# Kernel optimization log

Measured on AMD Instinct MI355X. Metric: run time of the kernel, lower is better.

The kernel has to match this reference:

```python
import jax, jax.numpy as jnp
import numpy as np

# Model dims
D = 2048        # hidden_size
H = 16          # num_heads
KVH = 8         # num_key_value_heads
DH = 128        # head_dim
NUM_SLOTS = 16  # state-cache slots
B = 4           # prefill segments (regularized ragged batch)
L = 2048        # tokens per segment
T = B * L
C = 64          # GLA chunk size (fused_chunk_gla)
NEG = -1e30


def setup_inputs() -> dict:
    key = jax.random.key(0)
    k0, k1, k2, k3 = jax.random.split(key, 4)
    hidden_states = jax.random.normal(k0, (T, D), jnp.float32)
    W_qkv = jax.random.normal(k1, (D, (H + 2 * KVH) * DH), jnp.float32) * 0.02
    b_qkv = jnp.zeros(((H + 2 * KVH) * DH,), jnp.float32)
    kv_cache = jax.random.normal(k2, (NUM_SLOTS, H, DH, DH), jnp.float32) * 0.1
    state_indices = jax.random.randint(k3, (B,), 0, NUM_SLOTS, jnp.int32)
    return {"hidden_states": hidden_states, "W_qkv": W_qkv, "b_qkv": b_qkv,
            "kv_cache": kv_cache, "state_indices": state_indices}


def _to_chunks(x):
    # [T, H, d] -> [n_chunks, B, C, H, d]
    return x.reshape(B, L // C, C, H, DH).transpose(1, 0, 2, 3, 4)


def _gla_chunk_body(mask):
    def body(S, inp):
        # S: [B,H,dk,dv]; qc/kc/vc/gc: [B,C,H,d]
        qc, kc, vc, gc = inp
        Bc = jnp.cumsum(gc, axis=1)                       # inclusive log-decay within chunk
        # inter-chunk: initial state decayed by exp(Bc)
        o_inter = jnp.einsum('bchk,bhkv->bchv', qc * jnp.exp(Bc), S)
        # intra-chunk causal scores: A_ij = sum_d q_i,d * exp(B_i - B_j)_d * k_j,d, j<=i
        diff = Bc[:, :, None] - Bc[:, None, :]            # [B,Ci,Cj,H,dk], <=0 on lower tri
        diff = jnp.where(mask[None, :, :, None, None], diff, NEG)
        A = jnp.einsum('bihk,bijhk,bjhk->bijh', qc, jnp.exp(diff), kc)
        o = o_inter + jnp.einsum('bijh,bjhv->bihv', A, vc)
        # state update: S' = diag(exp(B_last)) S + sum_j (k_j exp(B_last - B_j)) v_j^T
        b_last = Bc[:, -1]                                # [B,H,dk]
        kg = kc * jnp.exp(b_last[:, None] - Bc)
        S_new = S * jnp.exp(b_last)[..., None] + jnp.einsum('bchk,bchv->bhkv', kg, vc)
        return S_new, o
    return jax.checkpoint(body)


def _forward(hidden_states, W_qkv, b_qkv, kv_cache, state_indices):
    qkv = hidden_states @ W_qkv + b_qkv
    q = qkv[:, :H * DH].reshape(T, H, DH)
    k = qkv[:, H * DH:(H + KVH) * DH].reshape(T, KVH, DH)
    v = qkv[:, (H + KVH) * DH:].reshape(T, KVH, DH)
    n_rep = H // KVH
    k = jnp.repeat(k, n_rep, axis=1)                      # repeat_kv (3D branch)
    v = jnp.repeat(v, n_rep, axis=1)
    q = jax.nn.relu(q) * DH ** -0.5                       # q_feature_map + fused_chunk_gla scale
    k = jnp.minimum(jax.nn.sigmoid(k), 0.95)              # sigmoid + clamp(max=clamp_max)
    g = jnp.log1p(-k)                                     # (1 - k).log()

    S0 = kv_cache[state_indices]                          # [B,H,dk,dv] per-slot initial states
    mask = jnp.tril(jnp.ones((C, C), bool))
    _, o = jax.lax.scan(_gla_chunk_body(mask), S0,
                        (_to_chunks(q), _to_chunks(k), _to_chunks(v), _to_chunks(g)))
    # [n_chunks,B,C,H,dv] -> per-segment concat [T, H*dv]
    return o.transpose(1, 0, 2, 3, 4).reshape(T, H * DH)


def reference(hidden_states, W_qkv, b_qkv, kv_cache, state_indices):
    return _forward(hidden_states, W_qkv, b_qkv, kv_cache, state_indices)
```

## Files before the change

kernel.cpp:

```cpp
#include <hip/hip_runtime.h>
#include <hip/hip_bf16.h>
#include <math.h>

#define RSQRT_DH 0.08838834764831845f

typedef __attribute__((ext_vector_type(8))) short short8;
typedef __attribute__((ext_vector_type(4))) float floatx4;

static __device__ __forceinline__ float bf2f(unsigned short u) {
  return __uint_as_float(((unsigned int)u) << 16);
}
static __device__ __forceinline__ unsigned short f2bf(float f) {
  unsigned int x = __float_as_uint(f);
  return (unsigned short)((x + 0x7fffu + ((x >> 16) & 1u)) >> 16);
}
static __device__ __forceinline__ ushort4 f4bf(float a, float b, float c, float d) {
  ushort4 r; r.x = f2bf(a); r.y = f2bf(b); r.z = f2bf(c); r.w = f2bf(d); return r;
}
static __device__ __forceinline__ short8 ld8u(const unsigned short* p) {
  short4 a = *(const short4*)p;
  short4 b = *(const short4*)(p + 4);
  short8 r;
  r[0] = a.x; r[1] = a.y; r[2] = a.z; r[3] = a.w;
  r[4] = b.x; r[5] = b.y; r[6] = b.z; r[7] = b.w;
  return r;
}

__launch_bounds__(256)
__global__ void k_cvt(const float* __restrict__ in, unsigned short* __restrict__ out, int n4) {
  int i = blockIdx.x * 256 + threadIdx.x;
  if (i >= n4) return;
  float4 v = ((const float4*)in)[i];
  ((ushort4*)out)[i] = f4bf(v.x, v.y, v.z, v.w);
}

__launch_bounds__(256)
__global__ void k_cvt_wt(const float* __restrict__ W, unsigned short* __restrict__ Wt) {
  __shared__ float tile[32][33];
  int t = threadIdx.x;
  int c = t & 31, r = t >> 5;
  int bx = blockIdx.x, by = blockIdx.y;
#pragma unroll
  for (int j = 0; j < 4; ++j)
    tile[r + j * 8][c] = W[(size_t)(by * 32 + r + j * 8) * 4096 + bx * 32 + c];
  __syncthreads();
#pragma unroll
  for (int j = 0; j < 4; ++j)
    Wt[(size_t)(bx * 32 + r + j * 8) * 2048 + by * 32 + c] = f2bf(tile[c][r + j * 8]);
}

__launch_bounds__(256)
__global__ void k_gemm(const unsigned short* __restrict__ A,
                       const unsigned short* __restrict__ Bt,
                       const float* __restrict__ bias,
                       unsigned short* __restrict__ qb,
                       unsigned short* __restrict__ kb,
                       unsigned short* __restrict__ vb,
                       float* __restrict__ gf) {
  __shared__ unsigned short lds_a[128 * 64];
  __shared__ unsigned short lds_b[128 * 64];
  const int t = threadIdx.x;
  const int m0 = blockIdx.y * 128;
  const int n0 = blockIdx.x * 128;
  const int w = t >> 6, l = t & 63;
  const int wr = w >> 1, wc = w & 1;

  const int srow = l >> 3;
  const int scol = (l & 7) * 8;
  const unsigned short* agp = A + (size_t)(m0 + w * 8 + srow) * 2048 + scol;
  const unsigned short* bgp = Bt + (size_t)(n0 + w * 8 + srow) * 2048 + scol;

  floatx4 acc[4][4] = {};

  for (int kt = 0; kt < 2048; kt += 64) {
    __syncthreads();
#pragma unroll
    for (int it = 0; it < 4; ++it) {
      __builtin_amdgcn_global_load_lds(
          (const __attribute__((address_space(1))) void*)(agp + kt + (size_t)it * 32 * 2048),
          (__attribute__((address_space(3))) void*)(lds_a + (it * 32 + w * 8) * 64),
          16, 0, 0);
      __builtin_amdgcn_global_load_lds(
          (const __attribute__((address_space(1))) void*)(bgp + kt + (size_t)it * 32 * 2048),
          (__attribute__((address_space(3))) void*)(lds_b + (it * 32 + w * 8) * 64),
          16, 0, 0);
    }
    __syncthreads();
#pragma unroll
    for (int ks = 0; ks < 2; ++ks) {
      short8 af[4], bf[4];
      const int krow = ks * 32 + (l >> 4) * 8;
#pragma unroll
      for (int ti = 0; ti < 4; ++ti)
        af[ti] = *(const short8*)(lds_a + (wr * 64 + ti * 16 + (l & 15)) * 64 + krow);
#pragma unroll
      for (int tj = 0; tj < 4; ++tj)
        bf[tj] = *(const short8*)(lds_b + (wc * 64 + tj * 16 + (l & 15)) * 64 + krow);
#pragma unroll
      for (int ti = 0; ti < 4; ++ti)
#pragma unroll
        for (int tj = 0; tj < 4; ++tj)
          acc[ti][tj] = __builtin_amdgcn_mfma_f32_16x16x32_bf16(af[ti], bf[tj], acc[ti][tj], 0, 0, 0);
    }
  }
#pragma unroll
  for (int ti = 0; ti < 4; ++ti) {
#pragma unroll
    for (int tj = 0; tj < 4; ++tj) {
      const int n = n0 + wc * 64 + tj * 16 + (l & 15);
      const float bn = bias[n];
#pragma unroll
      for (int r = 0; r < 4; ++r) {
        const int m = m0 + wr * 64 + ti * 16 + ((l >> 4) * 4) + r;
        float val = acc[ti][tj][r] + bn;
        if (n < 2048) {
          qb[(size_t)m * 2048 + n] = f2bf(fmaxf(val, 0.f) * RSQRT_DH);
        } else if (n < 3072) {
          float s = 1.f / (1.f + __expf(-val));
          s = fminf(s, 0.95f);
          size_t idx = (size_t)m * 1024 + (n - 2048);
          kb[idx] = f2bf(s);
          gf[idx] = log1pf(-s);
        } else {
          vb[(size_t)m * 1024 + (n - 3072)] = f2bf(val);
        }
      }
    }
  }
}

__launch_bounds__(256)
__global__ void k_phaseA(const unsigned short* __restrict__ kb,
                         const unsigned short* __restrict__ vb,
                         const float* __restrict__ gf,
                         float* __restrict__ blast,
                         unsigned short* __restrict__ Pb) {
  __shared__ float sBc[64 * 128];
  __shared__ float sKg[64 * 128];
  const int t = threadIdx.x;
  const int chunk = blockIdx.x, chain = blockIdx.y;
  const int b = chain >> 4, h = chain & 15, kvh = h >> 1;
  const int t0 = b * 2048 + chunk * 64;

#pragma unroll
  for (int rep = 0; rep < 8; ++rep) {
    int e = rep * 256 + t;
    int i = e >> 5, d4 = e & 31;
    *(float4*)(sBc + i * 128 + d4 * 4) =
        *(const float4*)(gf + (size_t)(t0 + i) * 1024 + kvh * 128 + d4 * 4);
  }
  __syncthreads();
  if (t < 128) {
    float run = sBc[t];
    for (int i = 1; i < 64; ++i) { run += sBc[i * 128 + t]; sBc[i * 128 + t] = run; }
    blast[((size_t)chain * 32 + chunk) * 128 + t] = run;
  }
  __syncthreads();
#pragma unroll
  for (int rep = 0; rep < 32; ++rep) {
    int e = rep * 256 + t;
    int i = e >> 7, d = e & 127;
    float kk = bf2f(kb[(size_t)(t0 + i) * 1024 + kvh * 128 + d]);
    sKg[e] = kk * __expf(sBc[63 * 128 + d] - sBc[e]);
  }
  __syncthreads();
  const int kq = t >> 3, vq = t & 7;
  const int kd0 = kq * 4, vd0 = vq * 16;
  float acc[4][16] = {};
  const unsigned short* vrow = vb + (size_t)t0 * 1024 + kvh * 128 + vd0;
  for (int i = 0; i < 64; ++i) {
    float4 kg4 = *(const float4*)(sKg + i * 128 + kd0);
    float ka[4] = {kg4.x, kg4.y, kg4.z, kg4.w};
    ushort4 v0 = *(const ushort4*)(vrow + (size_t)i * 1024);
    ushort4 v1 = *(const ushort4*)(vrow + (size_t)i * 1024 + 4);
    ushort4 v2 = *(const ushort4*)(vrow + (size_t)i * 1024 + 8);
    ushort4 v3 = *(const ushort4*)(vrow + (size_t)i * 1024 + 12);
    float vf[16] = {bf2f(v0.x), bf2f(v0.y), bf2f(v0.z), bf2f(v0.w),
                    bf2f(v1.x), bf2f(v1.y), bf2f(v1.z), bf2f(v1.w),
                    bf2f(v2.x), bf2f(v2.y), bf2f(v2.z), bf2f(v2.w),
                    bf2f(v3.x), bf2f(v3.y), bf2f(v3.z), bf2f(v3.w)};
#pragma unroll
    for (int r = 0; r < 4; ++r)
#pragma unroll
      for (int j = 0; j < 16; ++j) acc[r][j] += ka[r] * vf[j];
  }
  size_t pbase = ((size_t)chain * 32 + chunk) * 16384;
#pragma unroll
  for (int r = 0; r < 4; ++r)
#pragma unroll
    for (int j4 = 0; j4 < 4; ++j4)
      *(ushort4*)(Pb + pbase + (size_t)(kd0 + r) * 128 + vd0 + j4 * 4) =
          f4bf(acc[r][j4 * 4], acc[r][j4 * 4 + 1], acc[r][j4 * 4 + 2], acc[r][j4 * 4 + 3]);
}

__launch_bounds__(256)
__global__ void k_scan(const float* __restrict__ kv_cache,
                       const int* __restrict__ sidx,
                       const float* __restrict__ blast,
                       const unsigned short* __restrict__ Pb,
                       unsigned short* __restrict__ Sb) {
  const int t = threadIdx.x;
  const int part = blockIdx.x;
  const int chain = blockIdx.y;
  const int b = chain >> 4, h = chain & 15;
  const int e0 = part * 1024 + t * 4;
  const int kd = e0 >> 7;
  const int slot = sidx[b];
  float4 s = *(const float4*)(kv_cache + ((size_t)slot * 16 + h) * 16384 + e0);
#pragma unroll 1
  for (int c = 0; c < 32; ++c) {
    *(ushort4*)(Sb + ((size_t)c * 64 + chain) * 16384 + e0) = f4bf(s.x, s.y, s.z, s.w);
    float eb = __expf(blast[((size_t)chain * 32 + c) * 128 + kd]);
    ushort4 p = *(const ushort4*)(Pb + ((size_t)chain * 32 + c) * 16384 + e0);
    s.x = s.x * eb + bf2f(p.x);
    s.y = s.y * eb + bf2f(p.y);
    s.z = s.z * eb + bf2f(p.z);
    s.w = s.w * eb + bf2f(p.w);
  }
}

__launch_bounds__(256)
__global__ void k_output(const unsigned short* __restrict__ qb,
                         const unsigned short* __restrict__ kb,
                         const unsigned short* __restrict__ vb,
                         const float* __restrict__ gf,
                         const unsigned short* __restrict__ Sb,
                         float* __restrict__ out) {
  __shared__ float sBc[64 * 128];
  __shared__ unsigned short sR3[11136];
  unsigned short* sA   = sR3;
  unsigned short* sKE  = sR3 + 4608;
  unsigned short* sQE2 = sR3 + 4608 + 4352;
  unsigned short* sQE0 = sR3;
  unsigned short* sSt  = sR3 + 4608;
  unsigned short* sVt  = sR3 + 4608;

  const int t = threadIdx.x;
  const int w = t >> 6, l = t & 63;
  const int lr = l & 15, quad = l >> 4;
  const int chunk = blockIdx.x, chain = blockIdx.y;
  const int b = chain >> 4, h = chain & 15, kvh = h >> 1;
  const int t0 = b * 2048 + chunk * 64;
  const size_t sbase = ((size_t)chunk * 64 + chain) * 16384;

#pragma unroll
  for (int rep = 0; rep < 8; ++rep) {
    int e = rep * 256 + t, i = e >> 5, d4 = e & 31;
    *(float4*)(sBc + i * 128 + d4 * 4) =
        *(const float4*)(gf + (size_t)(t0 + i) * 1024 + kvh * 128 + d4 * 4);
  }
  __syncthreads();
  if (t < 128) {
    float run = sBc[t];
#pragma unroll
    for (int i = 1; i < 64; ++i) { run += sBc[i * 128 + t]; sBc[i * 128 + t] = run; }
  }

  floatx4 o[8];
#pragma unroll
  for (int i = 0; i < 8; ++i) o[i] = 0.f;

#pragma unroll
  for (int kh = 0; kh < 2; ++kh) {
    __syncthreads();
#pragma unroll
    for (int rep = 0; rep < 2; ++rep) {
      int idx = rep * 256 + t;
      int i = idx >> 3, g = idx & 7;
      int k0 = kh * 64 + g * 8;
      short8 q8 = *(const short8*)(qb + (size_t)(t0 + i) * 2048 + h * 128 + k0);
      short8 r;
#pragma unroll
      for (int u = 0; u < 8; ++u)
        r[u] = (short)f2bf(bf2f((unsigned short)q8[u]) * __expf(sBc[i * 128 + k0 + u]));
      *(short8*)(sQE0 + i * 72 + g * 8) = r;
    }
#pragma unroll
    for (int vh = 0; vh < 2; ++vh) {
      __syncthreads();
#pragma unroll
      for (int rep = 0; rep < 2; ++rep) {
        int idx = rep * 256 + t;
        int kl = idx >> 3, g = idx & 7;
        short8 s8 = *(const short8*)(Sb + sbase + (size_t)(kh * 64 + kl) * 128 + vh * 64 + g * 8);
#pragma unroll
        for (int u = 0; u < 8; ++u) sSt[(g * 8 + u) * 76 + kl] = (unsigned short)s8[u];
      }
      __syncthreads();
      short8 af0 = *(const short8*)(sQE0 + (w * 16 + lr) * 72 + quad * 8);
      short8 af1 = *(const short8*)(sQE0 + (w * 16 + lr) * 72 + 32 + quad * 8);
#pragma unroll
      for (int tv = 0; tv < 4; ++tv) {
        const unsigned short* bp = sSt + (tv * 16 + lr) * 76 + quad * 8;
        short8 bf0 = ld8u(bp);
        short8 bf1 = ld8u(bp + 32);
        o[vh * 4 + tv] = __builtin_amdgcn_mfma_f32_16x16x32_bf16(af0, bf0, o[vh * 4 + tv], 0, 0, 0);
        o[vh * 4 + tv] = __builtin_amdgcn_mfma_f32_16x16x32_bf16(af1, bf1, o[vh * 4 + tv], 0, 0, 0);
      }
    }
  }

  __syncthreads();
  for (int idx = t; idx < 576; idx += 256)
    *(short8*)(sA + idx * 8) = (short8)0;
#pragma unroll
  for (int I = 0; I < 4; ++I) {
    const float* Rrow = (I > 0) ? (sBc + (I * 16 - 1) * 128) : nullptr;
    for (int base = 0; base < (I + 1) * 16; base += 32) {
      int nrows = min(32, (I + 1) * 16 - base);
      __syncthreads();
      int ngroups = nrows * 16;
      for (int idx = t; idx < ngroups; idx += 256) {
        int jl = idx >> 4, g = idx & 15;
        int j = base + jl, k0 = g * 8;
        short8 k8 = *(const short8*)(kb + (size_t)(t0 + j) * 1024 + kvh * 128 + k0);
        short8 r;
#pragma unroll
        for (int u = 0; u < 8; ++u) {
          int k = k0 + u;
          float Rk = Rrow ? Rrow[k] : 0.f;
          r[u] = (short)f2bf(bf2f((unsigned short)k8[u]) * __expf(Rk - sBc[j * 128 + k]));
        }
        *(short8*)(sKE + jl * 136 + k0) = r;
      }
      if (base == 0) {
        {
          int idx = t;
          int il = idx >> 4, g = idx & 15;
          int i = I * 16 + il, k0 = g * 8;
          short8 q8 = *(const short8*)(qb + (size_t)(t0 + i) * 2048 + h * 128 + k0);
          short8 r;
#pragma unroll
          for (int u = 0; u < 8; ++u) {
            int k = k0 + u;
            float Rk = Rrow ? Rrow[k] : 0.f;
            r[u] = (short)f2bf(bf2f((unsigned short)q8[u]) * __expf(sBc[i * 128 + k] - Rk));
          }
          *(short8*)(sQE2 + il * 136 + k0) = r;
        }
      }
      __syncthreads();
      const int J = w;
      if (J * 16 >= base && J * 16 < base + nrows) {
        floatx4 a4 = {};
#pragma unroll
        for (int ks = 0; ks < 4; ++ks) {
          short8 afr = *(const short8*)(sQE2 + lr * 136 + ks * 32 + quad * 8);
          short8 bfr = *(const short8*)(sKE + (J * 16 - base + lr) * 136 + ks * 32 + quad * 8);
          a4 = __builtin_amdgcn_mfma_f32_16x16x32_bf16(afr, bfr, a4, 0, 0, 0);
        }
#pragma unroll
        for (int r = 0; r < 4; ++r) {
          int il = quad * 4 + r;
          float v = ((J < I) || (lr <= il)) ? a4[r] : 0.f;
          sA[(I * 16 + il) * 72 + J * 16 + lr] = f2bf(v);
        }
      }
    }
  }

  __syncthreads();
  short8 aA0 = *(const short8*)(sA + (w * 16 + lr) * 72 + quad * 8);
  short8 aA1 = *(const short8*)(sA + (w * 16 + lr) * 72 + 32 + quad * 8);
#pragma unroll
  for (int vh = 0; vh < 2; ++vh) {
    if (vh) __syncthreads();
#pragma unroll
    for (int rep = 0; rep < 2; ++rep) {
      int idx = rep * 256 + t;
      int j = idx >> 3, g = idx & 7;
      short8 v8 = *(const short8*)(vb + (size_t)(t0 + j) * 1024 + kvh * 128 + vh * 64 + g * 8);
#pragma unroll
      for (int u = 0; u < 8; ++u) sVt[(g * 8 + u) * 76 + j] = (unsigned short)v8[u];
    }
    __syncthreads();
#pragma unroll
    for (int tv = 0; tv < 4; ++tv) {
      const unsigned short* bp = sVt + (tv * 16 + lr) * 76 + quad * 8;
      short8 b0 = ld8u(bp);
      short8 b1 = ld8u(bp + 32);
      o[vh * 4 + tv] = __builtin_amdgcn_mfma_f32_16x16x32_bf16(aA0, b0, o[vh * 4 + tv], 0, 0, 0);
      o[vh * 4 + tv] = __builtin_amdgcn_mfma_f32_16x16x32_bf16(aA1, b1, o[vh * 4 + tv], 0, 0, 0);
    }
  }

#pragma unroll
  for (int tv8 = 0; tv8 < 8; ++tv8) {
    int col = (tv8 >> 2) * 64 + (tv8 & 3) * 16 + lr;
#pragma unroll
    for (int r = 0; r < 4; ++r) {
      int i = w * 16 + quad * 4 + r;
      out[(size_t)(t0 + i) * 2048 + h * 128 + col] = o[tv8][r];
    }
  }
}

extern "C" void kernel_launch(void* const* d_in, const int* in_sizes, int n_in,
                              void* d_out, int out_size, void* d_ws, size_t ws_size,
                              hipStream_t stream) {
  (void)in_sizes; (void)n_in; (void)out_size; (void)ws_size;
  const float* hs   = (const float*)d_in[0];
  const float* W    = (const float*)d_in[1];
  const float* bias = (const float*)d_in[2];
  const float* kvc  = (const float*)d_in[3];
  const int*   sidx = (const int*)d_in[4];

  char* ws = (char*)d_ws;
  unsigned short* Sb  = (unsigned short*)(ws + 0);
  unsigned short* hsb = (unsigned short*)(ws + 0);
  unsigned short* wtb = (unsigned short*)(ws + 33554432);
  unsigned short* qb  = (unsigned short*)(ws + 67108864);
  unsigned short* kb  = (unsigned short*)(ws + 100663296);
  unsigned short* vb  = (unsigned short*)(ws + 117440512);
  float*          gf  = (float*)(ws + 134217728);
  float*          bl  = (float*)(ws + 167772160);
  unsigned short* Pb  = (unsigned short*)d_out;
  float* out = (float*)d_out;

  k_cvt<<<dim3(16384), dim3(256), 0, stream>>>(hs, hsb, 16777216 / 4);
  k_cvt_wt<<<dim3(128, 64), dim3(256), 0, stream>>>(W, wtb);
  k_gemm<<<dim3(32, 64), dim3(256), 0, stream>>>(hsb, wtb, bias, qb, kb, vb, gf);
  k_phaseA<<<dim3(32, 64), dim3(256), 0, stream>>>(kb, vb, gf, bl, Pb);
  k_scan<<<dim3(16, 64), dim3(256), 0, stream>>>(kvc, sidx, bl, Pb, Sb);
  k_output<<<dim3(32, 64), dim3(256), 0, stream>>>(qb, kb, vb, gf, Sb, out);
}
```

Before: 662.0 us.

## Swizzle GEMM LDS layout, remap blocks, stage epilogue via LDS, parallelize chunk cumsum

The QKV GEMM now stores its tiles in LDS with an XOR-swizzled 16-byte slot layout to avoid bank conflicts. It remaps the 1D block index to group tiles for better L2 locality, sets a launch-bounds occupancy hint, and routes accumulators through LDS so the epilogue writes coalesced 4-wide vectors. The serial 64-step per-column cumsum in phaseA and the output kernel is replaced by a log-step parallel scan across all 256 threads. The extra LDS round-trips and barriers in the epilogue and scan add synchronisation cost.

```diff
diff --git a/kernel.cpp b/kernel.cpp
--- a/kernel.cpp
+++ b/kernel.cpp
@@ -6,6 +6,8 @@
 
 typedef __attribute__((ext_vector_type(8))) short short8;
 typedef __attribute__((ext_vector_type(4))) float floatx4;
+
+#define MFMA16(a, b, c) __builtin_amdgcn_mfma_f32_16x16x32_bf16((a), (b), (c), 0, 0, 0)
 
 static __device__ __forceinline__ float bf2f(unsigned short u) {
   return __uint_as_float(((unsigned int)u) << 16);
@@ -49,7 +51,7 @@
     Wt[(size_t)(bx * 32 + r + j * 8) * 2048 + by * 32 + c] = f2bf(tile[c][r + j * 8]);
 }
 
-__launch_bounds__(256)
+__launch_bounds__(256, 4)
 __global__ void k_gemm(const unsigned short* __restrict__ A,
                        const unsigned short* __restrict__ Bt,
                        const float* __restrict__ bias,
@@ -57,75 +59,128 @@
                        unsigned short* __restrict__ kb,
                        unsigned short* __restrict__ vb,
                        float* __restrict__ gf) {
-  __shared__ unsigned short lds_a[128 * 64];
-  __shared__ unsigned short lds_b[128 * 64];
+  __shared__ unsigned short lds[16384];
+  char* lb = (char*)lds;
+
   const int t = threadIdx.x;
-  const int m0 = blockIdx.y * 128;
-  const int n0 = blockIdx.x * 128;
   const int w = t >> 6, l = t & 63;
   const int wr = w >> 1, wc = w & 1;
-
-  const int srow = l >> 3;
-  const int scol = (l & 7) * 8;
-  const unsigned short* agp = A + (size_t)(m0 + w * 8 + srow) * 2048 + scol;
-  const unsigned short* bgp = Bt + (size_t)(n0 + w * 8 + srow) * 2048 + scol;
+  const int lr = l & 15, quad = l >> 4;
+
+  const int id = blockIdx.x;
+  const int x = id & 7, loc = id >> 3;
+  const int bm = (x >> 1) * 16 + (loc >> 4);
+  const int bn = (x & 1) * 16 + (loc & 15);
+  const int m0 = bm * 128, n0 = bn * 128;
+
+  const int srow = t >> 3;
+  const int sslot = (t & 7) ^ (srow & 7);
+  const unsigned short* agp = A + (size_t)(m0 + srow) * 2048 + sslot * 8;
+  const unsigned short* bgp = Bt + (size_t)(n0 + srow) * 2048 + sslot * 8;
+
+  const int c16_0 = ((quad) ^ (lr & 7)) * 16;
+  const int c16_1 = ((4 + quad) ^ (lr & 7)) * 16;
+  const char* pA = lb + wr * 8192 + lr * 128;
+  const char* pB = lb + 16384 + wc * 8192 + lr * 128;
 
   floatx4 acc[4][4] = {};
 
-  for (int kt = 0; kt < 2048; kt += 64) {
+  for (int kt = 0; kt < 32; ++kt) {
     __syncthreads();
 #pragma unroll
     for (int it = 0; it < 4; ++it) {
       __builtin_amdgcn_global_load_lds(
-          (const __attribute__((address_space(1))) void*)(agp + kt + (size_t)it * 32 * 2048),
-          (__attribute__((address_space(3))) void*)(lds_a + (it * 32 + w * 8) * 64),
+          (const __attribute__((address_space(1))) void*)(agp + (size_t)it * 65536 + kt * 64),
+          (__attribute__((address_space(3))) void*)(lb + it * 4096 + t * 16),
           16, 0, 0);
       __builtin_amdgcn_global_load_lds(
-          (const __attribute__((address_space(1))) void*)(bgp + kt + (size_t)it * 32 * 2048),
-          (__attribute__((address_space(3))) void*)(lds_b + (it * 32 + w * 8) * 64),
+          (const __attribute__((address_space(1))) void*)(bgp + (size_t)it * 65536 + kt * 64),
+          (__attribute__((address_space(3))) void*)(lb + 16384 + it * 4096 + t * 16),
           16, 0, 0);
     }
     __syncthreads();
 #pragma unroll
     for (int ks = 0; ks < 2; ++ks) {
+      const int c16 = ks ? c16_1 : c16_0;
       short8 af[4], bf[4];
-      const int krow = ks * 32 + (l >> 4) * 8;
+#pragma unroll
+      for (int i = 0; i < 4; ++i) af[i] = *(const short8*)(pA + i * 2048 + c16);
+#pragma unroll
+      for (int i = 0; i < 4; ++i) bf[i] = *(const short8*)(pB + i * 2048 + c16);
 #pragma unroll
       for (int ti = 0; ti < 4; ++ti)
-        af[ti] = *(const short8*)(lds_a + (wr * 64 + ti * 16 + (l & 15)) * 64 + krow);
-#pragma unroll
-      for (int tj = 0; tj < 4; ++tj)
-        bf[tj] = *(const short8*)(lds_b + (wc * 64 + tj * 16 + (l & 15)) * 64 + krow);
-#pragma unroll
-      for (int ti = 0; ti < 4; ++ti)
 #pragma unroll
         for (int tj = 0; tj < 4; ++tj)
-          acc[ti][tj] = __builtin_amdgcn_mfma_f32_16x16x32_bf16(af[ti], bf[tj], acc[ti][tj], 0, 0, 0);
-    }
-  }
-#pragma unroll
-  for (int ti = 0; ti < 4; ++ti) {
-#pragma unroll
-    for (int tj = 0; tj < 4; ++tj) {
-      const int n = n0 + wc * 64 + tj * 16 + (l & 15);
-      const float bn = bias[n];
-#pragma unroll
-      for (int r = 0; r < 4; ++r) {
-        const int m = m0 + wr * 64 + ti * 16 + ((l >> 4) * 4) + r;
-        float val = acc[ti][tj][r] + bn;
-        if (n < 2048) {
-          qb[(size_t)m * 2048 + n] = f2bf(fmaxf(val, 0.f) * RSQRT_DH);
-        } else if (n < 3072) {
-          float s = 1.f / (1.f + __expf(-val));
-          s = fminf(s, 0.95f);
-          size_t idx = (size_t)m * 1024 + (n - 2048);
-          kb[idx] = f2bf(s);
-          gf[idx] = log1pf(-s);
-        } else {
-          vb[(size_t)m * 1024 + (n - 3072)] = f2bf(val);
-        }
-      }
-    }
+          acc[ti][tj] = MFMA16(af[ti], bf[tj], acc[ti][tj]);
+    }
+  }
+
+  float* ldsf = (float*)lds;
+  __syncthreads();
+
+  const int c4 = (t & 31) * 4;
+  float4 bv = *(const float4*)(bias + n0 + c4);
+
+#pragma unroll
+  for (int p = 0; p < 4; ++p) {
+#pragma unroll
+    for (int tj = 0; tj < 4; ++tj)
+#pragma unroll
+      for (int r = 0; r < 4; ++r)
+        ldsf[(wr * 16 + quad * 4 + r) * 132 + wc * 64 + tj * 16 + lr] = acc[p][tj][r];
+    __syncthreads();
+#pragma unroll
+    for (int it = 0; it < 4; ++it) {
+      const int row32 = it * 8 + (t >> 5);
+      const int grow = m0 + (row32 >> 4) * 64 + p * 16 + (row32 & 15);
+      float4 f = *(const float4*)&ldsf[row32 * 132 + c4];
+      f.x += bv.x; f.y += bv.y; f.z += bv.z; f.w += bv.w;
+      if (n0 < 2048) {
+        *(ushort4*)(qb + (size_t)grow * 2048 + n0 + c4) =
+            f4bf(fmaxf(f.x, 0.f) * RSQRT_DH, fmaxf(f.y, 0.f) * RSQRT_DH,
+                 fmaxf(f.z, 0.f) * RSQRT_DH, fmaxf(f.w, 0.f) * RSQRT_DH);
+      } else if (n0 < 3072) {
+        float sx = fminf(1.f / (1.f + __expf(-f.x)), 0.95f);
+        float sy = fminf(1.f / (1.f + __expf(-f.y)), 0.95f);
+        float sz = fminf(1.f / (1.f + __expf(-f.z)), 0.95f);
+        float sw = fminf(1.f / (1.f + __expf(-f.w)), 0.95f);
+        size_t idx = (size_t)grow * 1024 + (n0 - 2048) + c4;
+        *(ushort4*)(kb + idx) = f4bf(sx, sy, sz, sw);
+        float4 g4; g4.x = log1pf(-sx); g4.y = log1pf(-sy);
+        g4.z = log1pf(-sz); g4.w = log1pf(-sw);
+        *(float4*)(gf + idx) = g4;
+      } else {
+        *(ushort4*)(vb + (size_t)grow * 1024 + (n0 - 3072) + c4) =
+            f4bf(f.x, f.y, f.z, f.w);
+      }
+    }
+    __syncthreads();
+  }
+}
+
+static __device__ __forceinline__ void scan64x128(float* sBc, int t) {
+  float4* x4 = (float4*)sBc;
+#pragma unroll
+  for (int s = 1; s < 64; s <<= 1) {
+    const int off = s * 32;
+    float4 a[8];
+#pragma unroll
+    for (int j = 0; j < 8; ++j) {
+      int e = j * 256 + t;
+      if (e >= off) {
+        float4 cu = x4[e];
+        float4 pr = x4[e - off];
+        a[j].x = cu.x + pr.x; a[j].y = cu.y + pr.y;
+        a[j].z = cu.z + pr.z; a[j].w = cu.w + pr.w;
+      }
+    }
+    __syncthreads();
+#pragma unroll
+    for (int j = 0; j < 8; ++j) {
+      int e = j * 256 + t;
+      if (e >= off) x4[e] = a[j];
+    }
+    __syncthreads();
   }
 }
 
@@ -150,12 +205,8 @@
         *(const float4*)(gf + (size_t)(t0 + i) * 1024 + kvh * 128 + d4 * 4);
   }
   __syncthreads();
-  if (t < 128) {
-    float run = sBc[t];
-    for (int i = 1; i < 64; ++i) { run += sBc[i * 128 + t]; sBc[i * 128 + t] = run; }
-    blast[((size_t)chain * 32 + chunk) * 128 + t] = run;
-  }
-  __syncthreads();
+  scan64x128(sBc, t);
+  if (t < 128) blast[((size_t)chain * 32 + chunk) * 128 + t] = sBc[63 * 128 + t];
 #pragma unroll
   for (int rep = 0; rep < 32; ++rep) {
     int e = rep * 256 + t;
@@ -250,11 +301,7 @@
         *(const float4*)(gf + (size_t)(t0 + i) * 1024 + kvh * 128 + d4 * 4);
   }
   __syncthreads();
-  if (t < 128) {
-    float run = sBc[t];
-#pragma unroll
-    for (int i = 1; i < 64; ++i) { run += sBc[i * 128 + t]; sBc[i * 128 + t] = run; }
-  }
+  scan64x128(sBc, t);
 
   floatx4 o[8];
 #pragma unroll
@@ -294,8 +341,8 @@
         const unsigned short* bp = sSt + (tv * 16 + lr) * 76 + quad * 8;
         short8 bf0 = ld8u(bp);
         short8 bf1 = ld8u(bp + 32);
-        o[vh * 4 + tv] = __builtin_amdgcn_mfma_f32_16x16x32_bf16(af0, bf0, o[vh * 4 + tv], 0, 0, 0);
-        o[vh * 4 + tv] = __builtin_amdgcn_mfma_f32_16x16x32_bf16(af1, bf1, o[vh * 4 + tv], 0, 0, 0);
+        o[vh * 4 + tv] = MFMA16(af0, bf0, o[vh * 4 + tv]);
+        o[vh * 4 + tv] = MFMA16(af1, bf1, o[vh * 4 + tv]);
       }
     }
   }
@@ -347,7 +394,7 @@
         for (int ks = 0; ks < 4; ++ks) {
           short8 afr = *(const short8*)(sQE2 + lr * 136 + ks * 32 + quad * 8);
           short8 bfr = *(const short8*)(sKE + (J * 16 - base + lr) * 136 + ks * 32 + quad * 8);
-          a4 = __builtin_amdgcn_mfma_f32_16x16x32_bf16(afr, bfr, a4, 0, 0, 0);
+          a4 = MFMA16(afr, bfr, a4);
         }
 #pragma unroll
         for (int r = 0; r < 4; ++r) {
@@ -379,8 +426,8 @@
       const unsigned short* bp = sVt + (tv * 16 + lr) * 76 + quad * 8;
       short8 b0 = ld8u(bp);
       short8 b1 = ld8u(bp + 32);
-      o[vh * 4 + tv] = __builtin_amdgcn_mfma_f32_16x16x32_bf16(aA0, b0, o[vh * 4 + tv], 0, 0, 0);
-      o[vh * 4 + tv] = __builtin_amdgcn_mfma_f32_16x16x32_bf16(aA1, b1, o[vh * 4 + tv], 0, 0, 0);
+      o[vh * 4 + tv] = MFMA16(aA0, b0, o[vh * 4 + tv]);
+      o[vh * 4 + tv] = MFMA16(aA1, b1, o[vh * 4 + tv]);
     }
   }
 
@@ -419,7 +466,7 @@
 
   k_cvt<<<dim3(16384), dim3(256), 0, stream>>>(hs, hsb, 16777216 / 4);
   k_cvt_wt<<<dim3(128, 64), dim3(256), 0, stream>>>(W, wtb);
-  k_gemm<<<dim3(32, 64), dim3(256), 0, stream>>>(hsb, wtb, bias, qb, kb, vb, gf);
+  k_gemm<<<dim3(2048), dim3(256), 0, stream>>>(hsb, wtb, bias, qb, kb, vb, gf);
   k_phaseA<<<dim3(32, 64), dim3(256), 0, stream>>>(kb, vb, gf, bl, Pb);
   k_scan<<<dim3(16, 64), dim3(256), 0, stream>>>(kvc, sidx, bl, Pb, Sb);
   k_output<<<dim3(32, 64), dim3(256), 0, stream>>>(qb, kb, vb, gf, Sb, out);
```

After: 563.4 us. 1.18x faster.
